# Kernel tuning notes

Measured on AMD Instinct MI355X. Metric: run time of the kernel, lower is better.

## Reference

```python
import jax, jax.numpy as jnp
import numpy as np

NUM_HEADS = 16
NUM_BUCKETS = 32
MAX_DISTANCE = 128


def _rel_bucket(rel):
    # bidirectional T5-style relative position bucketing
    nb = NUM_BUCKETS // 2
    ret = (rel > 0).astype(jnp.int32) * nb
    n = jnp.abs(rel)
    max_exact = nb // 2
    is_small = n < max_exact
    safe = jnp.maximum(n, 1).astype(jnp.float32)
    large = max_exact + (jnp.log(safe / max_exact) / np.log(MAX_DISTANCE / max_exact) * (nb - max_exact)).astype(jnp.int32)
    large = jnp.minimum(large, nb - 1)
    return ret + jnp.where(is_small, n, large)


def setup_inputs() -> dict:
    key = jax.random.key(0)
    ks = jax.random.split(key, 12)
    S, B, E = 1024, 4, 1024
    D = E // NUM_HEADS
    s = 0.02
    return {
        "query": jax.random.normal(ks[0], (S, B, E), jnp.float32),
        "q_w": jax.random.normal(ks[1], (E, E), jnp.float32) * s,
        "q_b": jnp.zeros((E,), jnp.float32),
        "k_w": jax.random.normal(ks[2], (E, E), jnp.float32) * s,
        "k_b": jnp.zeros((E,), jnp.float32),
        "v_w": jax.random.normal(ks[3], (E, E), jnp.float32) * s,
        "v_b": jnp.zeros((E,), jnp.float32),
        "out_w": jax.random.normal(ks[4], (E, E), jnp.float32) * s,
        "out_b": jnp.zeros((E,), jnp.float32),
        "rel_emb": jax.random.normal(ks[5], (NUM_BUCKETS, NUM_HEADS), jnp.float32) * s,
        "grep_w": jax.random.normal(ks[6], (8, D), jnp.float32) * s,
        "grep_b": jnp.zeros((8,), jnp.float32),
        "grep_a": jnp.ones((NUM_HEADS,), jnp.float32),
    }


def reference(query, q_w, q_b, k_w, k_b, v_w, v_b, out_w, out_b, rel_emb, grep_w, grep_b, grep_a):
    S, B, E = query.shape
    H = NUM_HEADS
    D = E // H
    scaling = D ** -0.5

    q = (query @ q_w.T + q_b) * scaling  # scaling applied before gating, as in WavLM
    k = query @ k_w.T + k_b
    v = query @ v_w.T + v_b

    def split(x):  # (S,B,E) -> (B,H,S,D)
        return x.reshape(S, B, H, D).transpose(1, 2, 0, 3)

    q4, k4, v4 = split(q), split(k), split(v)

    attn = jnp.einsum('bhqd,bhkd->bhqk', q4, k4)  # (B,H,S,S)

    pos = jnp.arange(S)
    bucket = _rel_bucket(pos[None, :] - pos[:, None])  # (S,S)
    pbias = rel_emb[bucket].transpose(2, 0, 1)          # (H,S,S)

    # GRU-gated relative position scaling
    g = jnp.einsum('bhsd,ed->bhse', q4, grep_w) + grep_b      # (B,H,S,8)
    g = jax.nn.sigmoid(g.reshape(B, H, S, 2, 4).sum(-1))     # (B,H,S,2)
    gate_a, gate_b = g[..., 0], g[..., 1]
    gate = gate_a * (gate_b * grep_a[None, :, None] - 1.0) + 2.0  # (B,H,S)

    attn = attn + gate[..., None] * pbias[None]
    probs = jax.nn.softmax(attn, axis=-1)
    ctx = jnp.einsum('bhqk,bhkd->bhqd', probs, v4)  # (B,H,S,D)
    out = ctx.transpose(2, 0, 1, 3).reshape(S, B, E) @ out_w.T + out_b
    return out
```

## Files before the change

kernel.cpp:

```cpp
#include <hip/hip_runtime.h>
#include <hip/hip_bf16.h>
#include <stdint.h>


typedef short bf16x8 __attribute__((ext_vector_type(8)));
typedef _Float16 f16x8 __attribute__((ext_vector_type(8)));
typedef float f32x4 __attribute__((ext_vector_type(4)));
typedef float f32x16 __attribute__((ext_vector_type(16)));
typedef unsigned uint32x2 __attribute__((ext_vector_type(2)));

#define MFMA_BF16(a, b, c) __builtin_amdgcn_mfma_f32_16x16x32_bf16((a), (b), (c), 0, 0, 0)
#define MFMA_F16(a, b, c) __builtin_amdgcn_mfma_f32_16x16x32_f16((a), (b), (c), 0, 0, 0)
#define MFMA32_BF16(a, b, c) __builtin_amdgcn_mfma_f32_32x32x16_bf16((a), (b), (c), 0, 0, 0)

#define LOG2E 1.44269504088896f
#define LN2 0.693147180559945f

__device__ __forceinline__ unsigned short f2bf(float x) {
  union { float f; unsigned u; } v; v.f = x;
  unsigned r = v.u + 0x7fffu + ((v.u >> 16) & 1u);
  return (unsigned short)(r >> 16);
}
__device__ __forceinline__ float bf2f(unsigned short u) {
  union { unsigned u; float f; } v; v.u = ((unsigned)u) << 16;
  return v.f;
}
__device__ __forceinline__ unsigned short f2h(float x) {
  union { _Float16 h; unsigned short u; } v; v.h = (_Float16)x;
  return v.u;
}
__device__ __forceinline__ unsigned pk_bf2(float a, float b) {
  union { __hip_bfloat162 h2; unsigned u; } v;
  v.h2 = __float22bfloat162_rn(float2{a, b});
  return v.u;
}

__device__ __forceinline__ void gload_lds16(const void* g, void* l) {
  __builtin_amdgcn_global_load_lds(
      (const __attribute__((address_space(1))) unsigned int*)g,
      (__attribute__((address_space(3))) unsigned int*)l, 16, 0, 0);
}

__device__ __forceinline__ int swz(int row) { return (row ^ (row >> 2)) & 3; }

__global__ __launch_bounds__(256) void prep_kernel(
    const float* __restrict__ query, const float* __restrict__ q_w,
    const float* __restrict__ k_w, const float* __restrict__ v_w,
    const float* __restrict__ out_w, const float* __restrict__ rel_emb,
    unsigned short* __restrict__ q_bf, unsigned short* __restrict__ wq,
    unsigned short* __restrict__ wk, unsigned short* __restrict__ wv,
    unsigned short* __restrict__ ow_h,
    float* __restrict__ bias_f) {
  int i = blockIdx.x * 256 + threadIdx.x;
  if (i < 1048576) {
    int e4 = (i & 255) << 2;
    int sb = i >> 8;
    int s = sb >> 2, b = sb & 3;
    float4 q4 = *(const float4*)(query + ((size_t)i << 2));
    ushort4 o;
    o.x = f2bf(q4.x); o.y = f2bf(q4.y); o.z = f2bf(q4.z); o.w = f2bf(q4.w);
    *(ushort4*)&q_bf[((size_t)(b * 1024 + s) << 10) | e4] = o;
  } else if (i < 1310720) {
    int j = (i - 1048576) << 2;
    float4 a = *(const float4*)(q_w + j);
    float4 b = *(const float4*)(k_w + j);
    float4 c = *(const float4*)(v_w + j);
    float4 d = *(const float4*)(out_w + j);
    ushort4 o;
    o.x = f2bf(a.x); o.y = f2bf(a.y); o.z = f2bf(a.z); o.w = f2bf(a.w);
    *(ushort4*)&wq[j] = o;
    o.x = f2bf(b.x); o.y = f2bf(b.y); o.z = f2bf(b.z); o.w = f2bf(b.w);
    *(ushort4*)&wk[j] = o;
    o.x = f2bf(c.x); o.y = f2bf(c.y); o.z = f2bf(c.z); o.w = f2bf(c.w);
    *(ushort4*)&wv[j] = o;
    o.x = f2h(d.x); o.y = f2h(d.y); o.z = f2h(d.z); o.w = f2h(d.w);
    *(ushort4*)&ow_h[j] = o;
  } else {
    int idx = i - 1310720;
    if (idx >= 2056) return;
    if (idx >= 2047) {
#pragma unroll
      for (int h = 0; h < 16; ++h) bias_f[h * 2056 + idx] = 0.f;
      return;
    }
    int rel = idx - 1023;
    int n = rel < 0 ? -rel : rel;
    int ret = rel > 0 ? 16 : 0;
    int bucket;
    if (n < 8) {
      bucket = ret + n;
    } else {
      int large = 8 + (int)(logf((float)n / 8.0f) / logf(16.0f) * 8.0f);
      if (large > 15) large = 15;
      bucket = ret + large;
    }
#pragma unroll
    for (int h = 0; h < 16; ++h)
      bias_f[h * 2056 + idx] = rel_emb[bucket * 16 + h] * LOG2E;
  }
}

__global__ __launch_bounds__(256, 3) void qkv_gemm_kernel(
    const unsigned short* __restrict__ A, const unsigned short* __restrict__ Wq,
    const unsigned short* __restrict__ Wk, const unsigned short* __restrict__ Wv,
    const float* __restrict__ qb, const float* __restrict__ kb, const float* __restrict__ vb,
    unsigned short* __restrict__ qh,
    unsigned short* __restrict__ kh,
    unsigned short* __restrict__ vT)
{
  __shared__ __align__(16) char smem[32768];
  const int tid = threadIdx.x, lane = tid & 63;
  const int wv_ = tid >> 6;
  const int nt = blockIdx.x;
  const int mt = blockIdx.y;
  const int mat = nt >> 3;
  const unsigned short* W = mat == 0 ? Wq : (mat == 1 ? Wk : Wv);
  const int n0 = (nt & 7) * 128;
  const int m0 = mt * 128;
  const int moff = (wv_ & 1) * 64;
  const int noff = (wv_ >> 1) * 64;
  const int q15 = lane & 15, quad = lane >> 4;

  const int abase = (mat < 2) ? 8192 : 0;
  const int bbase2 = 8192 - abase;
  const int aoff = (mat < 2) ? noff : moff;
  const int boff = (mat < 2) ? moff : noff;

  f32x4 acc[4][4] = {};
  const char* Ab = (const char*)A;
  const char* Wb = (const char*)W;

  int st_row[2], st_g[2];
#pragma unroll
  for (int c = 0; c < 2; ++c) {
    int o = c * 4096 + tid * 16;
    int row = o >> 6, p = (o >> 4) & 3;
    st_row[c] = row;
    st_g[c] = p ^ swz(row);
  }

#define QKV_STAGE(kt, buf)                                                     \
  {                                                                            \
    char* bb = smem + (buf)*16384;                                             \
    _Pragma("unroll") for (int c = 0; c < 2; ++c) {                            \
      int o = c * 4096 + tid * 16;                                             \
      size_t ga = (size_t)(m0 + st_row[c]) * 2048 + (size_t)(kt)*64 + st_g[c] * 16; \
      size_t gb = (size_t)(n0 + st_row[c]) * 2048 + (size_t)(kt)*64 + st_g[c] * 16; \
      gload_lds16(Ab + ga, bb + o);                                            \
      gload_lds16(Wb + gb, bb + 8192 + o);                                     \
    }                                                                          \
  }

  QKV_STAGE(0, 0);
  for (int kt = 0; kt < 32; ++kt) {
    __syncthreads();
    const char* base = smem + (kt & 1) * 16384;
    if (kt < 31) QKV_STAGE(kt + 1, (kt + 1) & 1);

    bf16x8 af[4], bfr[4];
#pragma unroll
    for (int i = 0; i < 4; ++i) {
      int ra = aoff + i * 16 + q15;
      int rb = boff + i * 16 + q15;
      af[i] = *(const bf16x8*)(base + abase + ra * 64 + ((quad ^ swz(ra)) << 4));
      bfr[i] = *(const bf16x8*)(base + bbase2 + rb * 64 + ((quad ^ swz(rb)) << 4));
    }
#pragma unroll
    for (int i = 0; i < 4; ++i)
#pragma unroll
      for (int j = 0; j < 4; ++j) acc[i][j] = MFMA_BF16(af[i], bfr[j], acc[i][j]);
  }
#undef QKV_STAGE

  const int bidx = m0 >> 10;
  if (mat < 2) {
    const float* barr = mat == 0 ? qb : kb;
    unsigned short* dst = mat == 0 ? qh : kh;
    const float scale = mat == 0 ? (0.125f * LOG2E) : 1.0f;
    const int sA = (m0 & 1023) + moff + q15;
    const int nA = n0 + noff + (quad << 2);
#pragma unroll
    for (int i = 0; i < 4; ++i) {
      int colb = nA + i * 16;
      int hh = colb >> 6, dd = colb & 63;
      float bs0 = barr[colb + 0] * scale;
      float bs1 = barr[colb + 1] * scale;
      float bs2 = barr[colb + 2] * scale;
      float bs3 = barr[colb + 3] * scale;
#pragma unroll
      for (int j = 0; j < 4; ++j) {
        int s = sA + j * 16;
        ushort4 pk;
        pk.x = f2bf(__builtin_fmaf(acc[i][j][0], scale, bs0));
        pk.y = f2bf(__builtin_fmaf(acc[i][j][1], scale, bs1));
        pk.z = f2bf(__builtin_fmaf(acc[i][j][2], scale, bs2));
        pk.w = f2bf(__builtin_fmaf(acc[i][j][3], scale, bs3));
        *(ushort4*)&dst[((size_t)(bidx * 16 + hh) * 1024 + s) * 64 + dd] = pk;
      }
    }
  } else {
    const int s00 = (m0 & 1023) + moff + (quad << 2);
    const int c0 = n0 + noff + q15;
#pragma unroll
    for (int j = 0; j < 4; ++j) {
      int col = c0 + j * 16;
      int hh = col >> 6, dd = col & 63;
      float bias = vb[col];
#pragma unroll
      for (int i = 0; i < 4; ++i) {
        int s = s00 + i * 16;
        ushort4 pk;
        pk.x = f2bf(acc[i][j][0] + bias);
        pk.y = f2bf(acc[i][j][1] + bias);
        pk.z = f2bf(acc[i][j][2] + bias);
        pk.w = f2bf(acc[i][j][3] + bias);
        *(ushort4*)&vT[((size_t)(bidx * 16 + hh) * 64 + dd) * 1024 + s] = pk;
      }
    }
  }
}

__global__ __launch_bounds__(256) void gate_kernel(const unsigned short* __restrict__ qh,
                                                   const float* __restrict__ grep_w,
                                                   const float* __restrict__ grep_b,
                                                   const float* __restrict__ grep_a,
                                                   float* __restrict__ gate) {
  __shared__ float gw[512];
  __shared__ float gbb[8];
  __shared__ float gaa[16];
  int tid = threadIdx.x;
  for (int i = tid; i < 512; i += 256) gw[i] = grep_w[i];
  if (tid < 8) gbb[tid] = grep_b[tid];
  if (tid < 16) gaa[tid] = grep_a[tid];
  __syncthreads();
  int idx = blockIdx.x * 256 + tid;
  int h = (idx >> 10) & 15;
  const unsigned short* qrow = qh + (size_t)idx * 64;
  float a[8] = {0.f, 0.f, 0.f, 0.f, 0.f, 0.f, 0.f, 0.f};
#pragma unroll
  for (int c = 0; c < 8; ++c) {
    bf16x8 v = *(const bf16x8*)(qrow + c * 8);
#pragma unroll
    for (int jj = 0; jj < 8; ++jj) {
      float qv = bf2f((unsigned short)v[jj]);
      int d = c * 8 + jj;
#pragma unroll
      for (int e = 0; e < 8; ++e) a[e] += qv * gw[e * 64 + d];
    }
  }
  float sa = (a[0] + a[1] + a[2] + a[3]) * LN2 + gbb[0] + gbb[1] + gbb[2] + gbb[3];
  float sb = (a[4] + a[5] + a[6] + a[7]) * LN2 + gbb[4] + gbb[5] + gbb[6] + gbb[7];
  float siga = 1.f / (1.f + __expf(-sa));
  float sigb = 1.f / (1.f + __expf(-sb));
  gate[idx] = siga * (sigb * gaa[h] - 1.f) + 2.f;
}

__global__ __launch_bounds__(256, 4) void attn_kernel(
    const unsigned short* __restrict__ qh, const unsigned short* __restrict__ kh,
    const unsigned short* __restrict__ vT, const float* __restrict__ gate,
    const float* __restrict__ bias_f, unsigned short* __restrict__ ctx) {
  __shared__ __align__(16) char smem[37120];
  const int tid = threadIdx.x, lane = tid & 63, w = tid >> 6;
  const int qt = w >> 1, khalf = w & 1;
  const int bh = blockIdx.x;
  const int h = bh & 15;
  const int qs0 = blockIdx.y * 64;
  const int q31 = lane & 31, hb = lane >> 5, q7 = q31 & 7;
  const int sq = qs0 + qt * 32 + q31;

  float* bcf = (float*)(smem + 32768);
  {
    const float* gb = bias_f + h * 2056 + (960 - qs0);
    for (int i = tid; i < 1088; i += 256) bcf[i] = gb[i];
  }

  const char* kbase = (const char*)(kh + (size_t)bh * 65536);
  const char* vbase = (const char*)(vT + (size_t)bh * 65536);

  int o_[2];
  size_t koff_[2], voff_[2];
#pragma unroll
  for (int c = 0; c < 2; ++c) {
    int o = c * 4096 + tid * 16;
    int srow = o >> 7;
    int sg = ((o >> 4) & 7) ^ (srow & 7);
    o_[c] = o;
    koff_[c] = (size_t)srow * 128 + sg * 16;
    voff_[c] = (size_t)srow * 2048 + sg * 16;
  }

#define ATT_STAGE(kcn, buf)                                                          \
  {                                                                                  \
    _Pragma("unroll") for (int c = 0; c < 2; ++c) {                                  \
      gload_lds16(kbase + (size_t)(kcn)*8192 + koff_[c], smem + (buf)*8192 + o_[c]); \
      gload_lds16(vbase + (size_t)(kcn)*128 + voff_[c],                              \
                  smem + 16384 + (buf)*8192 + o_[c]);                                \
    }                                                                                \
  }

  ATT_STAGE(0, 0);

  const unsigned short* qrow = qh + ((size_t)bh * 1024 + sq) * 64 + hb * 8;
  bf16x8 qf[4];
#pragma unroll
  for (int dc = 0; dc < 4; ++dc) qf[dc] = *(const bf16x8*)(qrow + dc * 16);

  const float gate_lane = gate[bh * 1024 + sq];

  const int i0 = (qs0 + 63 - sq) + khalf * 32 + hb * 4;

  float l_run = 0.f;
  f32x16 accO0 = {}, accO1 = {};

  for (int kc = 0; kc < 16; ++kc) {
    __syncthreads();
    const char* Kc = smem + (kc & 1) * 8192;
    const char* Vc = smem + 16384 + (kc & 1) * 8192;
    if (kc < 15) ATT_STAGE(kc + 1, (kc + 1) & 1);

    f32x16 sac;
    {
      const int ib = i0 + kc * 64;
#pragma unroll
      for (int rg = 0; rg < 4; ++rg) {
        sac[rg * 4 + 0] = gate_lane * bcf[ib + rg * 8 + 0];
        sac[rg * 4 + 1] = gate_lane * bcf[ib + rg * 8 + 1];
        sac[rg * 4 + 2] = gate_lane * bcf[ib + rg * 8 + 2];
        sac[rg * 4 + 3] = gate_lane * bcf[ib + rg * 8 + 3];
      }
    }

    const char* Krow = Kc + (khalf * 32 + q31) * 128;
    __builtin_amdgcn_s_setprio(1);
#pragma unroll
    for (int ks = 0; ks < 4; ++ks) {
      bf16x8 kf = *(const bf16x8*)(Krow + (((ks * 2 + hb) ^ q7) << 4));
      sac = MFMA32_BF16(kf, qf[ks], sac);
    }
    __builtin_amdgcn_s_setprio(0);

    float ps = 0.f;
    unsigned pu[8];
#pragma unroll
    for (int rg = 0; rg < 4; ++rg) {
      float p0 = __builtin_exp2f(sac[rg * 4 + 0]);
      float p1 = __builtin_exp2f(sac[rg * 4 + 1]);
      float p2 = __builtin_exp2f(sac[rg * 4 + 2]);
      float p3 = __builtin_exp2f(sac[rg * 4 + 3]);
      ps += (p0 + p1) + (p2 + p3);
      pu[2 * rg] = pk_bf2(p0, p1);
      pu[2 * rg + 1] = pk_bf2(p2, p3);
    }
    l_run += ps;

    uint32x2 s02 = __builtin_amdgcn_permlane32_swap(pu[0], pu[2], false, false);
    uint32x2 s13 = __builtin_amdgcn_permlane32_swap(pu[1], pu[3], false, false);
    uint32x2 s46 = __builtin_amdgcn_permlane32_swap(pu[4], pu[6], false, false);
    uint32x2 s57 = __builtin_amdgcn_permlane32_swap(pu[5], pu[7], false, false);
    union PB { unsigned u[4]; bf16x8 v; } b0, b1;
    b0.u[0] = s02.x; b0.u[1] = s13.x; b0.u[2] = s02.y; b0.u[3] = s13.y;
    b1.u[0] = s46.x; b1.u[1] = s57.x; b1.u[2] = s46.y; b1.u[3] = s57.y;

    __builtin_amdgcn_s_setprio(1);
#pragma unroll
    for (int mf = 0; mf < 2; ++mf) {
      bf16x8 pb = mf ? b1.v : b0.v;
      int vch = ((khalf * 4 + mf * 2 + hb) ^ q7) << 4;
      bf16x8 v0f = *(const bf16x8*)(Vc + q31 * 128 + vch);
      bf16x8 v1f = *(const bf16x8*)(Vc + (32 + q31) * 128 + vch);
      accO0 = MFMA32_BF16(v0f, pb, accO0);
      accO1 = MFMA32_BF16(v1f, pb, accO1);
    }
    __builtin_amdgcn_s_setprio(0);
  }
#undef ATT_STAGE

  l_run += __shfl_xor(l_run, 32, 64);

  __syncthreads();
  float* Ot = (float*)smem;
  float* ow = Ot + (qt * 32 + q31) * 65;
  if (khalf == 0) {
#pragma unroll
    for (int rr = 0; rr < 16; ++rr) {
      int d = (rr & 3) + 8 * (rr >> 2) + 4 * hb;
      ow[d] = accO0[rr];
      ow[32 + d] = accO1[rr];
    }
    if (hb == 0) ow[64] = l_run;
  }
  __syncthreads();
  if (khalf == 1) {
    float inv = 1.0f / (ow[64] + l_run);
#pragma unroll
    for (int rr = 0; rr < 16; ++rr) {
      int d = (rr & 3) + 8 * (rr >> 2) + 4 * hb;
      ow[d] = (ow[d] + accO0[rr]) * inv;
      ow[32 + d] = (ow[32 + d] + accO1[rr]) * inv;
    }
  }
  __syncthreads();
  {
    int row = tid >> 2, dg = tid & 3;
    int s = qs0 + row;
    const float* src = Ot + row * 65 + dg * 16;
    unsigned short hbuf[16];
#pragma unroll
    for (int j = 0; j < 16; ++j) hbuf[j] = f2h(src[j]);
    size_t base = (size_t)(s * 4 + (bh >> 4)) * 1024 + h * 64 + dg * 16;
    *(uint4*)(ctx + base) = *(const uint4*)(hbuf);
    *(uint4*)(ctx + base + 8) = *(const uint4*)(hbuf + 8);
  }
}

__global__ __launch_bounds__(256, 3) void outproj_kernel(
    const unsigned short* __restrict__ Af,
    const unsigned short* __restrict__ Bf,
    const float* __restrict__ ob, float* __restrict__ out) {
  __shared__ __align__(16) char smem[24576];
  const int tid = threadIdx.x, lane = tid & 63, wv_ = tid >> 6;
  const int q15 = lane & 15, quad = lane >> 4;
  const int n0 = blockIdx.x * 128;
  const int m0 = blockIdx.y * 64;
  const int moff = (wv_ & 1) * 32;
  const int noff = (wv_ >> 1) * 64;

  const int oa = tid * 16;
  const int ra_ = oa >> 6;
  const int ga_ = (((oa >> 4) & 3) ^ swz(ra_)) << 4;
  int rb_[2], gb_[2], obo_[2];
#pragma unroll
  for (int c = 0; c < 2; ++c) {
    int ob2 = c * 4096 + tid * 16;
    obo_[c] = ob2;
    rb_[c] = ob2 >> 6;
    gb_[c] = (((ob2 >> 4) & 3) ^ swz(rb_[c])) << 4;
  }

#define OP_STAGE(kt, buf)                                                        \
  {                                                                              \
    char* bb = smem + (buf)*12288;                                               \
    size_t ga = (size_t)(m0 + ra_) * 2048 + (size_t)(kt)*64 + ga_;               \
    gload_lds16((const char*)Af + ga, bb + oa);                                  \
    _Pragma("unroll") for (int c = 0; c < 2; ++c) {                              \
      size_t gb = (size_t)(n0 + rb_[c]) * 2048 + (size_t)(kt)*64 + gb_[c];       \
      gload_lds16((const char*)Bf + gb, bb + 4096 + obo_[c]);                    \
    }                                                                            \
  }

  f32x4 acc[4][2] = {};
  OP_STAGE(0, 0);
  for (int kt = 0; kt < 32; ++kt) {
    __syncthreads();
    const char* base = smem + (kt & 1) * 12288;
    if (kt < 31) OP_STAGE(kt + 1, (kt + 1) & 1);

    f16x8 wf[4], cf[2];
#pragma unroll
    for (int i = 0; i < 4; ++i) {
      int rb = noff + i * 16 + q15;
      wf[i] = *(const f16x8*)(base + 4096 + rb * 64 + ((quad ^ swz(rb)) << 4));
    }
#pragma unroll
    for (int j = 0; j < 2; ++j) {
      int ra = moff + j * 16 + q15;
      cf[j] = *(const f16x8*)(base + ra * 64 + ((quad ^ swz(ra)) << 4));
    }
#pragma unroll
    for (int i = 0; i < 4; ++i)
#pragma unroll
      for (int j = 0; j < 2; ++j) acc[i][j] = MFMA_F16(wf[i], cf[j], acc[i][j]);
  }
#undef OP_STAGE

  const int sA = m0 + moff + q15;
  const int nA = n0 + noff + (quad << 2);
#pragma unroll
  for (int i = 0; i < 4; ++i) {
    int colb = nA + i * 16;
    float4 b4 = *(const float4*)&ob[colb];
#pragma unroll
    for (int j = 0; j < 2; ++j) {
      int s = sA + j * 16;
      float4 o4;
      o4.x = acc[i][j][0] + b4.x;
      o4.y = acc[i][j][1] + b4.y;
      o4.z = acc[i][j][2] + b4.z;
      o4.w = acc[i][j][3] + b4.w;
      *(float4*)&out[(size_t)s * 1024 + colb] = o4;
    }
  }
}

extern "C" void kernel_launch(void* const* d_in, const int* in_sizes, int n_in,
                              void* d_out, int out_size, void* d_ws, size_t ws_size,
                              hipStream_t stream) {
  const float* query = (const float*)d_in[0];
  const float* q_w = (const float*)d_in[1];
  const float* q_b = (const float*)d_in[2];
  const float* k_w = (const float*)d_in[3];
  const float* k_b = (const float*)d_in[4];
  const float* v_w = (const float*)d_in[5];
  const float* v_b = (const float*)d_in[6];
  const float* out_w = (const float*)d_in[7];
  const float* out_b = (const float*)d_in[8];
  const float* rel_emb = (const float*)d_in[9];
  const float* grep_w = (const float*)d_in[10];
  const float* grep_b = (const float*)d_in[11];
  const float* grep_a = (const float*)d_in[12];
  float* out = (float*)d_out;

  const size_t MB = 1u << 20;
  char* ws = (char*)d_ws;
  unsigned short* q_bf = (unsigned short*)(ws);
  unsigned short* wq_bf = (unsigned short*)(ws + 8 * MB);
  unsigned short* wk_bf = (unsigned short*)(ws + 10 * MB);
  unsigned short* wv_bf = (unsigned short*)(ws + 12 * MB);
  unsigned short* ow_h = (unsigned short*)(ws + 14 * MB);
  unsigned short* qhp = (unsigned short*)(ws + 16 * MB);
  unsigned short* khp = (unsigned short*)(ws + 24 * MB);
  unsigned short* vTp = (unsigned short*)(ws + 32 * MB);
  unsigned short* ctxp = (unsigned short*)(ws + 40 * MB);
  float* gatep = (float*)(ws + 48 * MB);
  float* biasp = (float*)(ws + 48 * MB + 256 * 1024);

  prep_kernel<<<5129, 256, 0, stream>>>(query, q_w, k_w, v_w, out_w, rel_emb, q_bf, wq_bf,
                                        wk_bf, wv_bf, ow_h, biasp);
  qkv_gemm_kernel<<<dim3(24, 32), 256, 0, stream>>>(q_bf, wq_bf, wk_bf, wv_bf, q_b, k_b, v_b,
                                                    qhp, khp, vTp);
  gate_kernel<<<256, 256, 0, stream>>>(qhp, grep_w, grep_b, grep_a, gatep);
  attn_kernel<<<dim3(64, 16), 256, 0, stream>>>(qhp, khp, vTp, gatep, biasp, ctxp);
  outproj_kernel<<<dim3(8, 64), 256, 0, stream>>>(ctxp, ow_h, out_b, out);
}
```

Baseline: 197.0 us.

## Software-pipeline attention loop so QK of next tile overlaps softmax·V of previous

Restructures the attention main loop into a two-stage software pipeline. The QK^T MFMA for chunk i runs alongside the exp/pack/PV of chunk i-1, using two score accumulators and a triple-buffered V ring in LDS. The intent is to hide the exp and permlane latency behind MFMA work. In exchange it uses more LDS and registers, so the launch bound drops from 4 to 3 blocks per CU, which may reduce occupancy.

```diff
diff --git a/kernel.cpp b/kernel.cpp
--- a/kernel.cpp
+++ b/kernel.cpp
@@ -255,11 +255,11 @@
   gate[idx] = siga * (sigb * gaa[h] - 1.f) + 2.f;
 }
 
-__global__ __launch_bounds__(256, 4) void attn_kernel(
+__global__ __launch_bounds__(256, 3) void attn_kernel(
     const unsigned short* __restrict__ qh, const unsigned short* __restrict__ kh,
     const unsigned short* __restrict__ vT, const float* __restrict__ gate,
     const float* __restrict__ bias_f, unsigned short* __restrict__ ctx) {
-  __shared__ __align__(16) char smem[37120];
+  __shared__ __align__(16) char smem[45312];
   const int tid = threadIdx.x, lane = tid & 63, w = tid >> 6;
   const int qt = w >> 1, khalf = w & 1;
   const int bh = blockIdx.x;
@@ -268,7 +268,7 @@
   const int q31 = lane & 31, hb = lane >> 5, q7 = q31 & 7;
   const int sq = qs0 + qt * 32 + q31;
 
-  float* bcf = (float*)(smem + 32768);
+  float* bcf = (float*)(smem + 40960);
   {
     const float* gb = bias_f + h * 2056 + (960 - qs0);
     for (int i = tid; i < 1088; i += 256) bcf[i] = gb[i];
@@ -289,16 +289,21 @@
     voff_[c] = (size_t)srow * 2048 + sg * 16;
   }
 
-#define ATT_STAGE(kcn, buf)                                                          \
-  {                                                                                  \
-    _Pragma("unroll") for (int c = 0; c < 2; ++c) {                                  \
-      gload_lds16(kbase + (size_t)(kcn)*8192 + koff_[c], smem + (buf)*8192 + o_[c]); \
-      gload_lds16(vbase + (size_t)(kcn)*128 + voff_[c],                              \
-                  smem + 16384 + (buf)*8192 + o_[c]);                                \
-    }                                                                                \
-  }
-
-  ATT_STAGE(0, 0);
+#define STAGE_K(kcn, dst)                                                \
+  { _Pragma("unroll") for (int c = 0; c < 2; ++c)                        \
+      gload_lds16(kbase + (size_t)(kcn)*8192 + koff_[c], (dst) + o_[c]); }
+#define STAGE_V(kcn, dst)                                                \
+  { _Pragma("unroll") for (int c = 0; c < 2; ++c)                        \
+      gload_lds16(vbase + (size_t)(kcn)*128 + voff_[c], (dst) + o_[c]); }
+
+  char* kb0 = smem;
+  char* kb1 = smem + 8192;
+  char* vcur = smem + 16384;
+  char* vnext = smem + 16384 + 8192;
+  char* vprev = smem + 16384 + 16384;
+
+  STAGE_K(0, kb0);
+  STAGE_V(0, vcur);
 
   const unsigned short* qrow = qh + ((size_t)bh * 1024 + sq) * 64 + hb * 8;
   bf16x8 qf[4];
@@ -311,69 +316,95 @@
 
   float l_run = 0.f;
   f32x16 accO0 = {}, accO1 = {};
-
-  for (int kc = 0; kc < 16; ++kc) {
+  f32x16 sacA, sacB;
+
+#define QK_PHASE(i, sac, kb)                                                  \
+  {                                                                           \
+    const int ib = i0 + (i)*64;                                               \
+    _Pragma("unroll") for (int rg = 0; rg < 4; ++rg) {                        \
+      sac[rg * 4 + 0] = gate_lane * bcf[ib + rg * 8 + 0];                     \
+      sac[rg * 4 + 1] = gate_lane * bcf[ib + rg * 8 + 1];                     \
+      sac[rg * 4 + 2] = gate_lane * bcf[ib + rg * 8 + 2];                     \
+      sac[rg * 4 + 3] = gate_lane * bcf[ib + rg * 8 + 3];                     \
+    }                                                                         \
+    const char* Krow = (kb) + (khalf * 32 + q31) * 128;                       \
+    __builtin_amdgcn_s_setprio(1);                                            \
+    _Pragma("unroll") for (int ks = 0; ks < 4; ++ks) {                        \
+      bf16x8 kf = *(const bf16x8*)(Krow + (((ks * 2 + hb) ^ q7) << 4));       \
+      sac = MFMA32_BF16(kf, qf[ks], sac);                                     \
+    }                                                                         \
+    __builtin_amdgcn_s_setprio(0);                                            \
+  }
+
+#define SMPV_PHASE(sac, vb)                                                   \
+  {                                                                           \
+    float ps = 0.f;                                                           \
+    unsigned pu[8];                                                           \
+    _Pragma("unroll") for (int rg = 0; rg < 4; ++rg) {                        \
+      float p0 = __builtin_exp2f(sac[rg * 4 + 0]);                            \
+      float p1 = __builtin_exp2f(sac[rg * 4 + 1]);                            \
+      float p2 = __builtin_exp2f(sac[rg * 4 + 2]);                            \
+      float p3 = __builtin_exp2f(sac[rg * 4 + 3]);                            \
+      ps += (p0 + p1) + (p2 + p3);                                            \
+      pu[2 * rg] = pk_bf2(p0, p1);                                            \
+      pu[2 * rg + 1] = pk_bf2(p2, p3);                                        \
+    }                                                                         \
+    l_run += ps;                                                              \
+    uint32x2 s02 = __builtin_amdgcn_permlane32_swap(pu[0], pu[2], false, false); \
+    uint32x2 s13 = __builtin_amdgcn_permlane32_swap(pu[1], pu[3], false, false); \
+    uint32x2 s46 = __builtin_amdgcn_permlane32_swap(pu[4], pu[6], false, false); \
+    uint32x2 s57 = __builtin_amdgcn_permlane32_swap(pu[5], pu[7], false, false); \
+    union PB { unsigned u[4]; bf16x8 v; } b0, b1;                             \
+    b0.u[0] = s02.x; b0.u[1] = s13.x; b0.u[2] = s02.y; b0.u[3] = s13.y;       \
+    b1.u[0] = s46.x; b1.u[1] = s57.x; b1.u[2] = s46.y; b1.u[3] = s57.y;       \
+    __builtin_amdgcn_s_setprio(1);                                            \
+    _Pragma("unroll") for (int mf = 0; mf < 2; ++mf) {                        \
+      bf16x8 pb = mf ? b1.v : b0.v;                                           \
+      int vch = ((khalf * 4 + mf * 2 + hb) ^ q7) << 4;                        \
+      bf16x8 v0f = *(const bf16x8*)((vb) + q31 * 128 + vch);                  \
+      bf16x8 v1f = *(const bf16x8*)((vb) + (32 + q31) * 128 + vch);           \
+      accO0 = MFMA32_BF16(v0f, pb, accO0);                                    \
+      accO1 = MFMA32_BF16(v1f, pb, accO1);                                    \
+    }                                                                         \
+    __builtin_amdgcn_s_setprio(0);                                            \
+  }
+
+#define VROT() { char* t = vprev; vprev = vcur; vcur = vnext; vnext = t; }
+
+  __syncthreads();
+  STAGE_K(1, kb1);
+  STAGE_V(1, vnext);
+  QK_PHASE(0, sacA, kb0);
+  VROT();
+
+  for (int k = 0; k < 7; ++k) {
+    const int i = 2 * k + 1;
     __syncthreads();
-    const char* Kc = smem + (kc & 1) * 8192;
-    const char* Vc = smem + 16384 + (kc & 1) * 8192;
-    if (kc < 15) ATT_STAGE(kc + 1, (kc + 1) & 1);
-
-    f32x16 sac;
-    {
-      const int ib = i0 + kc * 64;
-#pragma unroll
-      for (int rg = 0; rg < 4; ++rg) {
-        sac[rg * 4 + 0] = gate_lane * bcf[ib + rg * 8 + 0];
-        sac[rg * 4 + 1] = gate_lane * bcf[ib + rg * 8 + 1];
-        sac[rg * 4 + 2] = gate_lane * bcf[ib + rg * 8 + 2];
-        sac[rg * 4 + 3] = gate_lane * bcf[ib + rg * 8 + 3];
-      }
-    }
-
-    const char* Krow = Kc + (khalf * 32 + q31) * 128;
-    __builtin_amdgcn_s_setprio(1);
-#pragma unroll
-    for (int ks = 0; ks < 4; ++ks) {
-      bf16x8 kf = *(const bf16x8*)(Krow + (((ks * 2 + hb) ^ q7) << 4));
-      sac = MFMA32_BF16(kf, qf[ks], sac);
-    }
-    __builtin_amdgcn_s_setprio(0);
-
-    float ps = 0.f;
-    unsigned pu[8];
-#pragma unroll
-    for (int rg = 0; rg < 4; ++rg) {
-      float p0 = __builtin_exp2f(sac[rg * 4 + 0]);
-      float p1 = __builtin_exp2f(sac[rg * 4 + 1]);
-      float p2 = __builtin_exp2f(sac[rg * 4 + 2]);
-      float p3 = __builtin_exp2f(sac[rg * 4 + 3]);
-      ps += (p0 + p1) + (p2 + p3);
-      pu[2 * rg] = pk_bf2(p0, p1);
-      pu[2 * rg + 1] = pk_bf2(p2, p3);
-    }
-    l_run += ps;
-
-    uint32x2 s02 = __builtin_amdgcn_permlane32_swap(pu[0], pu[2], false, false);
-    uint32x2 s13 = __builtin_amdgcn_permlane32_swap(pu[1], pu[3], false, false);
-    uint32x2 s46 = __builtin_amdgcn_permlane32_swap(pu[4], pu[6], false, false);
-    uint32x2 s57 = __builtin_amdgcn_permlane32_swap(pu[5], pu[7], false, false);
-    union PB { unsigned u[4]; bf16x8 v; } b0, b1;
-    b0.u[0] = s02.x; b0.u[1] = s13.x; b0.u[2] = s02.y; b0.u[3] = s13.y;
-    b1.u[0] = s46.x; b1.u[1] = s57.x; b1.u[2] = s46.y; b1.u[3] = s57.y;
-
-    __builtin_amdgcn_s_setprio(1);
-#pragma unroll
-    for (int mf = 0; mf < 2; ++mf) {
-      bf16x8 pb = mf ? b1.v : b0.v;
-      int vch = ((khalf * 4 + mf * 2 + hb) ^ q7) << 4;
-      bf16x8 v0f = *(const bf16x8*)(Vc + q31 * 128 + vch);
-      bf16x8 v1f = *(const bf16x8*)(Vc + (32 + q31) * 128 + vch);
-      accO0 = MFMA32_BF16(v0f, pb, accO0);
-      accO1 = MFMA32_BF16(v1f, pb, accO1);
-    }
-    __builtin_amdgcn_s_setprio(0);
-  }
-#undef ATT_STAGE
+    STAGE_K(i + 1, kb0);
+    STAGE_V(i + 1, vnext);
+    QK_PHASE(i, sacB, kb1);
+    SMPV_PHASE(sacA, vprev);
+    VROT();
+    __syncthreads();
+    STAGE_K(i + 2, kb1);
+    STAGE_V(i + 2, vnext);
+    QK_PHASE(i + 1, sacA, kb0);
+    SMPV_PHASE(sacB, vprev);
+    VROT();
+  }
+
+  __syncthreads();
+  QK_PHASE(15, sacB, kb1);
+  SMPV_PHASE(sacA, vprev);
+  VROT();
+
+  SMPV_PHASE(sacB, vprev);
+
+#undef QK_PHASE
+#undef SMPV_PHASE
+#undef VROT
+#undef STAGE_K
+#undef STAGE_V
 
   l_run += __shfl_xor(l_run, 32, 64);
 
```

Measured after the change: 199.3 us. Within noise of the previous version (+1.2%).
